# Kernel tuning notes

Measured on AMD Instinct MI355X. Metric: run time of the kernel, lower is better.

The kernel has to match this reference:

```python
import jax, jax.numpy as jnp
import numpy as np

B, S, D, K = 8, 1024, 1024, 8192


def setup_inputs() -> dict:
    key = jax.random.key(0)
    k1, k2 = jax.random.split(key)
    z = jax.random.normal(k1, (B, S, D), dtype=jnp.float32)
    codebook = jax.random.normal(k2, (K, D), dtype=jnp.float32)
    return {"z": z, "codebook": codebook}


def reference(z, codebook):
    # Eval-mode forward of VectorQuantizer (no EMA / dead-code side effects).
    b, s, d = z.shape
    z_flat = z.reshape(-1, d)                              # [N, D]
    # squared L2 distances: ||z||^2 + ||e||^2 - 2 z.e
    distances = (jnp.sum(z_flat * z_flat, axis=1, keepdims=True)
                 + jnp.sum(codebook * codebook, axis=1)
                 - 2.0 * jnp.einsum('nd,kd->nk', z_flat, codebook))  # [N, K]
    indices = jnp.argmin(distances, axis=1)                # [N]
    quantized = codebook[indices].reshape(b, s, d)         # gather
    loss = jnp.asarray(0.0, dtype=z.dtype)                 # eval mode
    # straight-through estimator
    quantized = z + jax.lax.stop_gradient(quantized - z)
    logits = -distances.reshape(b, s, -1)                  # [B, S, K]
    return quantized, indices.reshape(b, s), loss, logits
```

## Files before the change

### kernel.cpp

```cpp
#include <hip/hip_runtime.h>
#include <hip/hip_bf16.h>
#include <stdint.h>

#define NROWS 8192
#define KCODES 8192
#define DDIM 1024

#define Q_OFF    0
#define IDX_OFF  8388608
#define LOSS_OFF 8396800
#define LOG_OFF  8396801

using f32x4  = __attribute__((ext_vector_type(4))) float;
using i32x4  = __attribute__((ext_vector_type(4))) int;

__device__ __forceinline__ unsigned int forder(float f) {
  unsigned int u = __float_as_uint(f);
  return (u & 0x80000000u) ? ~u : (u | 0x80000000u);
}
__device__ __forceinline__ float finv(unsigned int u) {
  return (u & 0x80000000u) ? __uint_as_float(u & 0x7fffffffu) : __uint_as_float(~u);
}

__device__ __forceinline__ void gld_lds16(const void* g, void* l) {
  __builtin_amdgcn_global_load_lds((const __attribute__((address_space(1))) unsigned int*)g,
                                   (__attribute__((address_space(3))) unsigned int*)l,
                                   16, 0, 0);
}

__global__ __launch_bounds__(256) void vq_convert(const float* __restrict__ z,
                                                  const float* __restrict__ cb,
                                                  signed char* __restrict__ qbuf,
                                                  float* __restrict__ nrm,
                                                  float* __restrict__ scl,
                                                  unsigned int* __restrict__ gmins) {
  const int r = blockIdx.x;
  const int tid = threadIdx.x;
  if (r < 1024) gmins[r * 256 + tid] = 0xFFFFFFFFu;

  const float* src = (r < NROWS) ? (z + (size_t)r * DDIM)
                                 : (cb + (size_t)(r - NROWS) * DDIM);
  float4 v = reinterpret_cast<const float4*>(src)[tid];
  float vv[4] = {v.x, v.y, v.z, v.w};

  float amax = fmaxf(fmaxf(fabsf(vv[0]), fabsf(vv[1])),
                     fmaxf(fabsf(vv[2]), fabsf(vv[3])));
  float ss = vv[0]*vv[0] + vv[1]*vv[1] + vv[2]*vv[2] + vv[3]*vv[3];
  #pragma unroll
  for (int m = 32; m > 0; m >>= 1) {
    amax = fmaxf(amax, __shfl_down(amax, m, 64));
    ss += __shfl_down(ss, m, 64);
  }
  __shared__ float rA[4], rS[4], sB;
  if ((tid & 63) == 0) { rA[tid >> 6] = amax; rS[tid >> 6] = ss; }
  __syncthreads();
  if (tid == 0) {
    const float a = fmaxf(fmaxf(rA[0], rA[1]), fmaxf(rA[2], rA[3]));
    nrm[r] = rS[0] + rS[1] + rS[2] + rS[3];
    const float s = fmaxf(a, 1e-20f) * (1.0f / 127.0f);
    scl[r] = s;
    sB = s;
  }
  __syncthreads();
  const float inv = 1.0f / sB;
  int q[4];
  #pragma unroll
  for (int j = 0; j < 4; ++j) {
    int t = (int)rintf(vv[j] * inv);
    q[j] = t < -127 ? -127 : (t > 127 ? 127 : t);
  }
  const int packed = (q[0] & 255) | ((q[1] & 255) << 8) |
                     ((q[2] & 255) << 16) | (q[3] << 24);
  reinterpret_cast<int*>(qbuf + (size_t)r * DDIM)[tid] = packed;
}

__global__ __launch_bounds__(512, 2) void vq_mfma(const signed char* __restrict__ zq,
                                                  const signed char* __restrict__ cq,
                                                  const float* __restrict__ nrm,
                                                  const float* __restrict__ scl,
                                                  unsigned int* __restrict__ gmins,
                                                  float* __restrict__ out) {
  __shared__ i32x4 lds[3072];

  const int wgid = blockIdx.x;
  const int stx = wgid & 7;
  const int idx = wgid >> 3;
  const int sty = idx >> 5;
  const int tt_ = idx & 31;
  const int bx = stx * 4 + (tt_ & 3);
  const int by = sty * 8 + (tt_ >> 2);

  const int k0 = bx * 256;
  const int n0 = by * 128;
  const int tid = threadIdx.x;
  const int wid = tid >> 6, lane = tid & 63;
  const int wm = wid >> 2, wn = wid & 3;
  const int l15 = lane & 15, l4 = lane >> 4;

  const signed char* gaA;
  const signed char* gb[2];
  int ldstA, ldstB[2];
  {
    const int rowA = wid * 16 + (lane >> 2);
    const int cgA = (lane & 3) ^ ((rowA >> 1) & 3);
    gaA = zq + (size_t)(n0 + rowA) * DDIM + cgA * 16;
    ldstA = wid * 1024;
  }
  #pragma unroll
  for (int q = 0; q < 2; ++q) {
    const int s = wid * 2 + q;
    const int row = s * 16 + (lane >> 2);
    const int cg = (lane & 3) ^ ((row >> 1) & 3);
    gb[q] = cq + (size_t)(k0 + row) * DDIM + cg * 16;
    ldstB[q] = s * 1024;
  }

  auto stage = [&](int t, int b) {
    const int d0 = t * 64;
    gld_lds16(gaA + d0, (char*)lds + b * 24576 + ldstA);
    #pragma unroll
    for (int q = 0; q < 2; ++q)
      gld_lds16(gb[q] + d0, (char*)lds + b * 24576 + 8192 + ldstB[q]);
  };

  i32x4 acc[4][4];
  #pragma unroll
  for (int i = 0; i < 4; ++i)
    #pragma unroll
    for (int j = 0; j < 4; ++j) acc[i][j] = (i32x4){0, 0, 0, 0};

  stage(0, 0);
  asm volatile("s_waitcnt vmcnt(0)" ::: "memory");
  __builtin_amdgcn_s_barrier();

  #pragma unroll 2
  for (int t = 0; t < 16; ++t) {
    const int cur = t & 1;
    if (t < 15) stage(t + 1, cur ^ 1);
    const int base = cur * 1536;
    i32x4 af[4], bf[4];
    #pragma unroll
    for (int f = 0; f < 4; ++f) {
      const int ar = wm * 64 + f * 16 + l15;
      af[f] = lds[base + ar * 4 + (l4 ^ ((ar >> 1) & 3))];
      const int br = wn * 64 + f * 16 + l15;
      bf[f] = lds[base + 512 + br * 4 + (l4 ^ ((br >> 1) & 3))];
    }
    asm volatile("s_waitcnt lgkmcnt(0)" ::: "memory");
    __builtin_amdgcn_sched_barrier(0);
    __builtin_amdgcn_s_setprio(1);
    #pragma unroll
    for (int fm = 0; fm < 4; ++fm)
      #pragma unroll
      for (int fn = 0; fn < 4; ++fn)
        acc[fm][fn] = __builtin_amdgcn_mfma_i32_16x16x64_i8(af[fm], bf[fn], acc[fm][fn], 0, 0, 0);
    __builtin_amdgcn_s_setprio(0);
    if (t < 15) {
      asm volatile("s_waitcnt vmcnt(0)" ::: "memory");
      __builtin_amdgcn_s_barrier();
    }
  }

  float ee[4], sk[4];
  #pragma unroll
  for (int j = 0; j < 4; ++j) {
    const int kk = k0 + wn * 64 + j * 16 + l15;
    ee[j] = nrm[NROWS + kk];
    sk[j] = scl[NROWS + kk];
  }

  float* logits = out + LOG_OFF;
  #pragma unroll
  for (int f = 0; f < 4; ++f) {
    #pragma unroll
    for (int r = 0; r < 4; ++r) {
      const int n = n0 + wm * 64 + f * 16 + l4 * 4 + r;
      const float zz = nrm[n];
      const float sn2 = -2.0f * scl[n];
      float rowmin = 3.4e38f;
      #pragma unroll
      for (int j = 0; j < 4; ++j) {
        const int k = k0 + wn * 64 + j * 16 + l15;
        const float dist = fmaf(sn2 * sk[j], (float)acc[f][j][r], zz + ee[j]);
        logits[(size_t)n * KCODES + k] = -dist;
        rowmin = fminf(rowmin, dist);
      }
      #pragma unroll
      for (int mm = 1; mm < 16; mm <<= 1)
        rowmin = fminf(rowmin, __shfl_xor(rowmin, mm, 64));
      if (l15 == 0) atomicMin(&gmins[(size_t)n * 32 + bx], forder(rowmin));
    }
  }
}

#define MARGIN 16.0f
__global__ __launch_bounds__(256) void vq_refine(const float* __restrict__ z,
                                                 const float* __restrict__ cb,
                                                 const float* __restrict__ nrm,
                                                 const unsigned int* __restrict__ gmins,
                                                 float* __restrict__ out) {
  const int n = blockIdx.x;
  const int tid = threadIdx.x;
  __shared__ float tminS[32];
  __shared__ float gminS;
  __shared__ int cnt;
  __shared__ int cand[64];
  __shared__ float red[4];

  if (tid < 32) tminS[tid] = finv(gmins[(size_t)n * 32 + tid]);
  if (tid == 0) cnt = 0;
  __syncthreads();
  if (tid == 0) {
    float g = tminS[0];
    #pragma unroll
    for (int i = 1; i < 32; ++i) g = fminf(g, tminS[i]);
    gminS = g;
  }
  __syncthreads();
  const float thr = gminS + MARGIN;

  const float* lrow = out + LOG_OFF + (size_t)n * KCODES;
  for (int g = 0; g < 32; ++g) {
    if (tminS[g] <= thr) {
      const float dist = -lrow[g * 256 + tid];
      if (dist <= thr) {
        const int p = atomicAdd(&cnt, 1);
        if (p < 64) cand[p] = g * 256 + tid;
      }
    }
  }
  __syncthreads();
  const int ncand = min(cnt, 64);

  const float zz = nrm[n];
  const float4 zv = reinterpret_cast<const float4*>(z + (size_t)n * DDIM)[tid];
  float bestd = 0.f;
  int bestk = -1;
  for (int ci = 0; ci < ncand; ++ci) {
    const int k = cand[ci];
    const float4 ev = reinterpret_cast<const float4*>(cb + (size_t)k * DDIM)[tid];
    float s = zv.x * ev.x + zv.y * ev.y + zv.z * ev.z + zv.w * ev.w;
    #pragma unroll
    for (int mm = 32; mm > 0; mm >>= 1) s += __shfl_down(s, mm, 64);
    if ((tid & 63) == 0) red[tid >> 6] = s;
    __syncthreads();
    const float dot = red[0] + red[1] + red[2] + red[3];
    const float dist = zz + nrm[NROWS + k] - 2.0f * dot;
    if (bestk < 0 || dist < bestd || (dist == bestd && k < bestk)) {
      bestd = dist; bestk = k;
    }
    __syncthreads();
  }

  const float4* src = reinterpret_cast<const float4*>(cb + (size_t)bestk * DDIM);
  float4* dst = reinterpret_cast<float4*>(out + (size_t)n * DDIM);
  dst[tid] = src[tid];
  if (tid == 0) {
    out[IDX_OFF + n] = (float)bestk;
    if (n == 0) out[LOSS_OFF] = 0.f;
  }
}

extern "C" void kernel_launch(void* const* d_in, const int* in_sizes, int n_in,
                              void* d_out, int out_size, void* d_ws, size_t ws_size,
                              hipStream_t stream) {
  const float* z  = (const float*)d_in[0];
  const float* cb = (const float*)d_in[1];
  float* out = (float*)d_out;

  float* nrm = (float*)d_ws;
  float* scl = (float*)((char*)d_ws + 65536);
  unsigned int* gmins = (unsigned int*)((char*)d_ws + 131072);

  signed char* qbuf = (signed char*)out;
  const signed char* zq = qbuf;
  const signed char* cq = qbuf + (size_t)NROWS * DDIM;

  vq_convert<<<NROWS + KCODES, 256, 0, stream>>>(z, cb, qbuf, nrm, scl, gmins);
  vq_mfma<<<2048, 512, 0, stream>>>(zq, cq, nrm, scl, gmins, out);
  vq_refine<<<NROWS, 256, 0, stream>>>(z, cb, nrm, gmins, out);
}
```

Before: 193.3 us.

## Enlarge int8 MFMA tile to 256x256 with 1024-thread workgroups

Doubles the row tile of the int8 distance GEMM from 128 to 256 rows per workgroup, using 16 waves (1024 threads) and one workgroup per CU. Each wave now stages one A and one B 16-row slab per k-step, and the LDS double buffer grows to 64 KB. The aim is more reuse of each staged codebook tile and fewer global loads per MFMA. In exchange there are half as many workgroups, occupancy drops to one block per CU, and barriers now synchronise more waves. The epilogue must still map the wider tile correctly.

```diff
diff --git a/kernel.cpp b/kernel.cpp
--- a/kernel.cpp
+++ b/kernel.cpp
@@ -74,53 +74,37 @@
   reinterpret_cast<int*>(qbuf + (size_t)r * DDIM)[tid] = packed;
 }
 
-__global__ __launch_bounds__(512, 2) void vq_mfma(const signed char* __restrict__ zq,
-                                                  const signed char* __restrict__ cq,
-                                                  const float* __restrict__ nrm,
-                                                  const float* __restrict__ scl,
-                                                  unsigned int* __restrict__ gmins,
-                                                  float* __restrict__ out) {
-  __shared__ i32x4 lds[3072];
+__global__ __launch_bounds__(1024, 1) void vq_mfma(const signed char* __restrict__ zq,
+                                                   const signed char* __restrict__ cq,
+                                                   const float* __restrict__ nrm,
+                                                   const float* __restrict__ scl,
+                                                   unsigned int* __restrict__ gmins,
+                                                   float* __restrict__ out) {
+  __shared__ i32x4 lds[4096];
 
   const int wgid = blockIdx.x;
   const int stx = wgid & 7;
   const int idx = wgid >> 3;
-  const int sty = idx >> 5;
-  const int tt_ = idx & 31;
-  const int bx = stx * 4 + (tt_ & 3);
-  const int by = sty * 8 + (tt_ >> 2);
+  const int bx = stx * 4 + (idx & 3);
+  const int by = idx >> 2;
 
   const int k0 = bx * 256;
-  const int n0 = by * 128;
+  const int n0 = by * 256;
   const int tid = threadIdx.x;
   const int wid = tid >> 6, lane = tid & 63;
   const int wm = wid >> 2, wn = wid & 3;
   const int l15 = lane & 15, l4 = lane >> 4;
 
-  const signed char* gaA;
-  const signed char* gb[2];
-  int ldstA, ldstB[2];
-  {
-    const int rowA = wid * 16 + (lane >> 2);
-    const int cgA = (lane & 3) ^ ((rowA >> 1) & 3);
-    gaA = zq + (size_t)(n0 + rowA) * DDIM + cgA * 16;
-    ldstA = wid * 1024;
-  }
-  #pragma unroll
-  for (int q = 0; q < 2; ++q) {
-    const int s = wid * 2 + q;
-    const int row = s * 16 + (lane >> 2);
-    const int cg = (lane & 3) ^ ((row >> 1) & 3);
-    gb[q] = cq + (size_t)(k0 + row) * DDIM + cg * 16;
-    ldstB[q] = s * 1024;
-  }
+  const int srow = wid * 16 + (lane >> 2);
+  const int scg = (lane & 3) ^ ((srow >> 1) & 3);
+  const signed char* gaA = zq + (size_t)(n0 + srow) * DDIM + scg * 16;
+  const signed char* gbB = cq + (size_t)(k0 + srow) * DDIM + scg * 16;
+  const int ldst = wid * 1024;
 
   auto stage = [&](int t, int b) {
     const int d0 = t * 64;
-    gld_lds16(gaA + d0, (char*)lds + b * 24576 + ldstA);
-    #pragma unroll
-    for (int q = 0; q < 2; ++q)
-      gld_lds16(gb[q] + d0, (char*)lds + b * 24576 + 8192 + ldstB[q]);
+    gld_lds16(gaA + d0, (char*)lds + b * 32768 + ldst);
+    gld_lds16(gbB + d0, (char*)lds + b * 32768 + 16384 + ldst);
   };
 
   i32x4 acc[4][4];
@@ -137,14 +121,14 @@
   for (int t = 0; t < 16; ++t) {
     const int cur = t & 1;
     if (t < 15) stage(t + 1, cur ^ 1);
-    const int base = cur * 1536;
+    const int base = cur * 2048;
     i32x4 af[4], bf[4];
     #pragma unroll
     for (int f = 0; f < 4; ++f) {
       const int ar = wm * 64 + f * 16 + l15;
       af[f] = lds[base + ar * 4 + (l4 ^ ((ar >> 1) & 3))];
       const int br = wn * 64 + f * 16 + l15;
-      bf[f] = lds[base + 512 + br * 4 + (l4 ^ ((br >> 1) & 3))];
+      bf[f] = lds[base + 1024 + br * 4 + (l4 ^ ((br >> 1) & 3))];
     }
     asm volatile("s_waitcnt lgkmcnt(0)" ::: "memory");
     __builtin_amdgcn_sched_barrier(0);
@@ -277,6 +261,6 @@
   const signed char* cq = qbuf + (size_t)NROWS * DDIM;
 
   vq_convert<<<NROWS + KCODES, 256, 0, stream>>>(z, cb, qbuf, nrm, scl, gmins);
-  vq_mfma<<<2048, 512, 0, stream>>>(zq, cq, nrm, scl, gmins, out);
+  vq_mfma<<<1024, 1024, 0, stream>>>(zq, cq, nrm, scl, gmins, out);
   vq_refine<<<NROWS, 256, 0, stream>>>(z, cb, nrm, gmins, out);
 }
```

Result: no change. 189.8 us (-1.8%).
